# Performance work log

Measured on AMD Instinct MI355X. Metric: run time of the kernel, lower is better.

The kernel has to match this reference:

```python
import jax, jax.numpy as jnp
import numpy as np

K = 3          # kernel size
PAD = 1
STRIDE = 1
CIN = 256
COUT = 256


def _offset_conv(x, w, b):
    # standard 3x3 conv, NCHW / OIHW
    y = jax.lax.conv_general_dilated(
        x, w, window_strides=(STRIDE, STRIDE),
        padding=((PAD, PAD), (PAD, PAD)),
        dimension_numbers=("NCHW", "OIHW", "NCHW"))
    return y + b[None, :, None, None]


def _deform_conv2d(x, offset, weight):
    # x: [B,C,H,W], offset: [B,2*K*K,Ho,Wo] (y,x pairs, torchvision layout),
    # weight: [Cout,Cin,K,K]. No mask (deform-conv v1), zero padding.
    B, C, H, W = x.shape
    KK = K * K
    Ho, Wo = offset.shape[2], offset.shape[3]
    off = offset.reshape(B, KK, 2, Ho, Wo)
    dy, dx = off[:, :, 0], off[:, :, 1]                     # [B,KK,Ho,Wo]

    ky = jnp.repeat(jnp.arange(K), K).astype(x.dtype)       # [KK] kernel row
    kx = jnp.tile(jnp.arange(K), K).astype(x.dtype)         # [KK] kernel col
    base_y = (jnp.arange(Ho) * STRIDE - PAD).astype(x.dtype)
    base_x = (jnp.arange(Wo) * STRIDE - PAD).astype(x.dtype)

    py = base_y[None, None, :, None] + ky[None, :, None, None] + dy  # [B,KK,Ho,Wo]
    px = base_x[None, None, None, :] + kx[None, :, None, None] + dx

    y0 = jnp.floor(py); x0 = jnp.floor(px)
    y1 = y0 + 1.0;      x1 = x0 + 1.0
    wy1 = py - y0; wy0 = 1.0 - wy1
    wx1 = px - x0; wx0 = 1.0 - wx1

    xf = x.reshape(B, C, H * W)

    def gather(yi, xi):
        valid = ((yi >= 0) & (yi < H) & (xi >= 0) & (xi < W)).astype(x.dtype)
        yc = jnp.clip(yi, 0, H - 1).astype(jnp.int32)
        xc = jnp.clip(xi, 0, W - 1).astype(jnp.int32)
        idx = (yc * W + xc).reshape(B, -1)                  # [B, KK*Ho*Wo]
        v = jax.vmap(lambda xb, ib: xb[:, ib])(xf, idx)     # [B,C,KK*Ho*Wo]
        return v.reshape(B, C, KK, Ho, Wo), valid

    v00, m00 = gather(y0, x0)
    v01, m01 = gather(y0, x1)
    v10, m10 = gather(y1, x0)
    v11, m11 = gather(y1, x1)

    samp = (v00 * (wy0 * wx0 * m00)[:, None]
          + v01 * (wy0 * wx1 * m01)[:, None]
          + v10 * (wy1 * wx0 * m10)[:, None]
          + v11 * (wy1 * wx1 * m11)[:, None])               # [B,C,KK,Ho,Wo]

    w2 = weight.reshape(weight.shape[0], C, KK)             # [Cout,Cin,KK], KK=ky*K+kx
    return jnp.einsum('bckhw,ock->bohw', samp, w2)


def setup_inputs() -> dict:
    key = jax.random.key(0)
    k1, k2, k3, k4 = jax.random.split(key, 4)
    x = jax.random.normal(k1, (4, CIN, 64, 64), dtype=jnp.float32)
    # offset conv params (small init so sampled offsets are realistic)
    offset_w = jax.random.normal(k2, (2 * K * K, CIN, K, K), dtype=jnp.float32) * 0.01
    offset_b = jax.random.normal(k3, (2 * K * K,), dtype=jnp.float32) * 0.01
    # regular (deformable) conv weight; bias=False in the module
    weight = jax.random.normal(k4, (COUT, CIN, K, K), dtype=jnp.float32) * (1.0 / np.sqrt(CIN * K * K))
    return {"x": x, "offset_w": offset_w, "offset_b": offset_b, "weight": weight}


def reference(x, offset_w, offset_b, weight):
    offset = _offset_conv(x, offset_w, offset_b)
    return _deform_conv2d(x, offset, weight)
```

## Files before the change

### kernel.cpp

```cpp
#include <hip/hip_runtime.h>

#define CIN 256
#define COUT 256
#define Hh 64
#define Ww 64
#define Bb 4
#define HW 4096
#define NKK 9

typedef __attribute__((ext_vector_type(8))) short bf16x8;
typedef __attribute__((ext_vector_type(4))) float f32x4;

__device__ __forceinline__ unsigned short f2bf(float f) {
  unsigned int u = __builtin_bit_cast(unsigned int, f);
  unsigned int r = u + 0x7FFFu + ((u >> 16) & 1u);
  return (unsigned short)(r >> 16);
}
__device__ __forceinline__ float bf2f(unsigned short h) {
  unsigned int u = ((unsigned int)h) << 16;
  return __builtin_bit_cast(float, u);
}
__device__ __forceinline__ float bil(float2 f0, float2 f1, int eq, float4 w) {
  float t00 = eq ? f0.x : f0.y;
  float t01 = eq ? f0.y : f0.x;
  float t10 = eq ? f1.x : f1.y;
  float t11 = eq ? f1.y : f1.x;
  return t00 * w.x + t01 * w.y + t10 * w.z + t11 * w.w;
}

#define WB_ELEMS 589824
#define WOB_ELEMS 147456
#define OFFPART_FLOATS (Bb * 18 * HW)

__global__ __launch_bounds__(256) void prep_weights_kernel(
    const float* __restrict__ w, const float* __restrict__ ow,
    unsigned short* __restrict__ wBh, unsigned short* __restrict__ wBl,
    unsigned short* __restrict__ wOBh) {
  int i = blockIdx.x * 256 + threadIdx.x;
  if (i < WB_ELEMS) {
    int e = i & 7;
    int lane = (i >> 3) & 63;
    int ks = (i >> 9) & 1;
    int nt = (i >> 10) & 15;
    int cb = (i >> 14) & 3;
    int kk = i >> 16;
    int c = cb * 64 + ks * 32 + (lane >> 4) * 8 + e;
    int oc = nt * 16 + (lane & 15);
    float v = w[((size_t)oc * CIN + c) * 9 + kk];
    unsigned short hi = f2bf(v);
    wBh[i] = hi;
    wBl[i] = f2bf(v - bf2f(hi));
  } else {
    int j = i - WB_ELEMS;
    if (j < WOB_ELEMS) {
      int e = j & 7;
      int lane = (j >> 3) & 63;
      int ks = (j >> 9) & 1;
      int nt = (j >> 10) & 1;
      int cb = (j >> 11) & 3;
      int kk = j >> 13;
      int c = cb * 64 + ks * 32 + (lane >> 4) * 8 + e;
      int oc = nt * 16 + (lane & 15);
      float v = (oc < 18) ? ow[((size_t)oc * CIN + c) * 9 + kk] : 0.0f;
      wOBh[j] = f2bf(v);
    }
  }
}

__global__ __launch_bounds__(256) void offset_conv_kernel(
    const float* __restrict__ x,
    const unsigned short* __restrict__ wOBh,
    const float* __restrict__ ob,
    float* __restrict__ op0, float* __restrict__ op1) {
  __shared__ __align__(16) unsigned short smA[64 * 64];

  const int tid = threadIdx.x;
  const int bid = blockIdx.x;
  const int logical = (bid & 7) * 64 + (bid >> 3);
  const int chalf = logical & 1;
  const int rowid = logical >> 1;
  const int ho = rowid & 63;
  const int b  = rowid >> 6;
  const int lane = tid & 63;
  const int wv = tid >> 6;
  const int px = tid & 63;
  const int c8g = tid >> 6;

  f32x4 acc[2];
  #pragma unroll
  for (int n = 0; n < 2; ++n)
    #pragma unroll
    for (int q = 0; q < 4; ++q) acc[n][q] = 0.0f;

  const float* xb = x + (size_t)b * CIN * HW;

  for (int kk = 0; kk < NKK; ++kk) {
    int ky = kk / 3, kx = kk % 3;
    int y = ho - 1 + ky;
    if (y < 0 || y >= Hh) continue;
    int xx = px - 1 + kx;
    bool xv = (xx >= 0 && xx < Ww);
    int xxc = min(max(xx, 0), Ww - 1);
    const float* xrow = xb + (size_t)y * Ww + xxc;
    #pragma unroll
    for (int cb2 = 0; cb2 < 2; ++cb2) {
      int cb = chalf * 2 + cb2;
      __syncthreads();
      #pragma unroll
      for (int pass = 0; pass < 2; ++pass) {
        int c8 = c8g * 2 + pass;
        int cbase = cb * 64 + c8 * 8;
        unsigned int ph[4];
        #pragma unroll
        for (int j = 0; j < 4; ++j) {
          float v0 = xv ? xrow[(size_t)(cbase + 2 * j) * HW] : 0.0f;
          float v1 = xv ? xrow[(size_t)(cbase + 2 * j + 1) * HW] : 0.0f;
          ph[j] = (unsigned int)f2bf(v0) | ((unsigned int)f2bf(v1) << 16);
        }
        int boff = px * 128 + ((c8 ^ (px & 7)) * 16);
        *(uint4*)((char*)smA + boff) = make_uint4(ph[0], ph[1], ph[2], ph[3]);
      }
      __syncthreads();
      bf16x8 a[2];
      #pragma unroll
      for (int ks = 0; ks < 2; ++ks) {
        int pxa = wv * 16 + (lane & 15);
        int cg = ks * 4 + (lane >> 4);
        a[ks] = *(const bf16x8*)((const char*)smA + pxa * 128 + ((cg ^ (pxa & 7)) * 16));
      }
      bf16x8 wb[2][2];
      #pragma unroll
      for (int nt = 0; nt < 2; ++nt)
        #pragma unroll
        for (int ks = 0; ks < 2; ++ks) {
          size_t wi = ((((size_t)(kk * 4 + cb) * 2 + nt) * 2 + ks) * 64 + lane) * 8;
          wb[nt][ks] = *(const bf16x8*)(wOBh + wi);
        }
      #pragma unroll
      for (int nt = 0; nt < 2; ++nt)
        #pragma unroll
        for (int ks = 0; ks < 2; ++ks)
          acc[nt] = __builtin_amdgcn_mfma_f32_16x16x32_bf16(a[ks], wb[nt][ks], acc[nt], 0, 0, 0);
    }
  }
  float* opart = chalf ? op1 : op0;
  #pragma unroll
  for (int nt = 0; nt < 2; ++nt) {
    int oc = nt * 16 + (lane & 15);
    if (oc < 18) {
      float bias = chalf ? 0.0f : ob[oc];
      float4 v4 = make_float4(acc[nt][0] + bias, acc[nt][1] + bias,
                              acc[nt][2] + bias, acc[nt][3] + bias);
      int pxo = wv * 16 + (lane >> 4) * 4;
      *(float4*)(opart + ((size_t)b * 18 + oc) * HW + (size_t)ho * Ww + pxo) = v4;
    }
  }
}

__global__ __launch_bounds__(512, 2) void deform_main_kernel(
    const float* __restrict__ x,
    const float* __restrict__ op0, const float* __restrict__ op1,
    const unsigned short* __restrict__ wBh, const unsigned short* __restrict__ wBl,
    float* __restrict__ out) {
  __shared__ __align__(16) int4   sm_m[NKK][64];
  __shared__ __align__(16) float4 sm_w[NKK][64];
  __shared__ __align__(16) unsigned short smAh[2][64 * 64];
  __shared__ __align__(16) unsigned short smAl[2][64 * 64];

  const int tid = threadIdx.x;
  const int bid = blockIdx.x;
  const int blk = (bid & 7) * 32 + (bid >> 3);
  const int ho = blk & 63;
  const int b  = blk >> 6;
  const int lane = tid & 63;
  const int wv = tid >> 6;
  const int mh = wv >> 2;
  const int og = wv & 3;

  const float* ob0 = op0 + (size_t)b * 18 * HW + (size_t)ho * Ww;
  const float* ob1 = op1 + (size_t)b * 18 * HW + (size_t)ho * Ww;
  for (int i = tid; i < NKK * 64; i += 512) {
    int pp = i & 63;
    int kk = i >> 6;
    int ky = kk / 3, kx = kk % 3;
    float dy = ob0[(size_t)(2 * kk) * HW + pp] + ob1[(size_t)(2 * kk) * HW + pp];
    float dx = ob0[(size_t)(2 * kk + 1) * HW + pp] + ob1[(size_t)(2 * kk + 1) * HW + pp];
    float py = (float)(ho - 1 + ky) + dy;
    float pxf = (float)(pp - 1 + kx) + dx;
    float y0f = floorf(py), x0f = floorf(pxf);
    int y0 = (int)y0f, x0 = (int)x0f;
    float wy1 = py - y0f, wy0 = 1.0f - wy1;
    float wx1 = pxf - x0f, wx0 = 1.0f - wx1;
    float vy0 = (y0 >= 0 && y0 < Hh) ? 1.0f : 0.0f;
    float vy1 = (y0 + 1 >= 0 && y0 + 1 < Hh) ? 1.0f : 0.0f;
    float vx0 = (x0 >= 0 && x0 < Ww) ? 1.0f : 0.0f;
    float vx1 = (x0 + 1 >= 0 && x0 + 1 < Ww) ? 1.0f : 0.0f;
    int y0c = min(max(y0, 0), Hh - 1);
    int y1c = min(max(y0 + 1, 0), Hh - 1);
    int x0c = min(max(x0, 0), Ww - 2);
    int eq = (x0 == x0c) ? 1 : 0;
    sm_m[kk][pp] = make_int4(y0c * Ww + x0c, y1c * Ww + x0c, eq, 0);
    sm_w[kk][pp] = make_float4(wy0 * wx0 * vy0 * vx0, wy0 * wx1 * vy0 * vx1,
                               wy1 * wx0 * vy1 * vx0, wy1 * wx1 * vy1 * vx1);
  }
  __syncthreads();

  f32x4 acc[2][4];
  #pragma unroll
  for (int m = 0; m < 2; ++m)
    #pragma unroll
    for (int n = 0; n < 4; ++n)
      #pragma unroll
      for (int q = 0; q < 4; ++q) acc[m][n][q] = 0.0f;

  const float* xb = x + (size_t)b * CIN * HW;
  const int spx = tid & 63;
  const int sc8 = tid >> 6;
  const int sboff = spx * 128 + ((sc8 ^ (spx & 7)) * 16);

  {
    int4 ip = sm_m[0][spx];
    float4 wp = sm_w[0][spx];
    const float* xpB = xb + (size_t)(sc8 * 8) * HW;
    float2 g0[8], g1[8];
    #pragma unroll
    for (int j = 0; j < 8; ++j) {
      const float* xp = xpB + (size_t)j * HW;
      g0[j] = *(const float2*)(xp + ip.x);
      g1[j] = *(const float2*)(xp + ip.y);
    }
    unsigned int ph[4], pl[4];
    #pragma unroll
    for (int j2 = 0; j2 < 4; ++j2) {
      float v0 = bil(g0[2 * j2], g1[2 * j2], ip.z, wp);
      float v1 = bil(g0[2 * j2 + 1], g1[2 * j2 + 1], ip.z, wp);
      unsigned short h0 = f2bf(v0), h1 = f2bf(v1);
      ph[j2] = (unsigned int)h0 | ((unsigned int)h1 << 16);
      pl[j2] = (unsigned int)f2bf(v0 - bf2f(h0)) | ((unsigned int)f2bf(v1 - bf2f(h1)) << 16);
    }
    *(uint4*)((char*)smAh[0] + sboff) = make_uint4(ph[0], ph[1], ph[2], ph[3]);
    *(uint4*)((char*)smAl[0] + sboff) = make_uint4(pl[0], pl[1], pl[2], pl[3]);
  }
  __syncthreads();

  for (int ch = 0; ch < 36; ++ch) {
    const int cur = ch & 1;
    const int kk = ch >> 2, cb = ch & 3;

    bf16x8 ah[2][2], al[2][2];
    #pragma unroll
    for (int m = 0; m < 2; ++m)
      #pragma unroll
      for (int ks = 0; ks < 2; ++ks) {
        int pxa = mh * 32 + m * 16 + (lane & 15);
        int cg = ks * 4 + (lane >> 4);
        int aoff = pxa * 128 + ((cg ^ (pxa & 7)) * 16);
        ah[m][ks] = *(const bf16x8*)((const char*)smAh[cur] + aoff);
        al[m][ks] = *(const bf16x8*)((const char*)smAl[cur] + aoff);
      }

    bf16x8 wh[4][2], wl[4][2];
    #pragma unroll
    for (int nt = 0; nt < 4; ++nt)
      #pragma unroll
      for (int ks = 0; ks < 2; ++ks) {
        size_t wi = ((((size_t)(kk * 4 + cb) * 16 + (og * 4 + nt)) * 2 + ks) * 64 + lane) * 8;
        wh[nt][ks] = *(const bf16x8*)(wBh + wi);
        wl[nt][ks] = *(const bf16x8*)(wBl + wi);
      }
    asm volatile("" ::: "memory");

    float2 g0[8], g1[8];
    int4 ipn; float4 wpn;
    const bool have_next = (ch + 1 < 36);
    if (have_next) {
      int kkn = (ch + 1) >> 2, cbn = (ch + 1) & 3;
      ipn = sm_m[kkn][spx];
      wpn = sm_w[kkn][spx];
      const float* xpB = xb + (size_t)(cbn * 64 + sc8 * 8) * HW;
      #pragma unroll
      for (int j = 0; j < 8; ++j) {
        const float* xp = xpB + (size_t)j * HW;
        g0[j] = *(const float2*)(xp + ipn.x);
        g1[j] = *(const float2*)(xp + ipn.y);
      }
    }

    #pragma unroll
    for (int nt = 0; nt < 4; ++nt)
      #pragma unroll
      for (int ks = 0; ks < 2; ++ks) {
        acc[0][nt] = __builtin_amdgcn_mfma_f32_16x16x32_bf16(ah[0][ks], wh[nt][ks], acc[0][nt], 0, 0, 0);
        acc[1][nt] = __builtin_amdgcn_mfma_f32_16x16x32_bf16(ah[1][ks], wh[nt][ks], acc[1][nt], 0, 0, 0);
        acc[0][nt] = __builtin_amdgcn_mfma_f32_16x16x32_bf16(al[0][ks], wh[nt][ks], acc[0][nt], 0, 0, 0);
        acc[1][nt] = __builtin_amdgcn_mfma_f32_16x16x32_bf16(al[1][ks], wh[nt][ks], acc[1][nt], 0, 0, 0);
        acc[0][nt] = __builtin_amdgcn_mfma_f32_16x16x32_bf16(ah[0][ks], wl[nt][ks], acc[0][nt], 0, 0, 0);
        acc[1][nt] = __builtin_amdgcn_mfma_f32_16x16x32_bf16(ah[1][ks], wl[nt][ks], acc[1][nt], 0, 0, 0);
      }

    if (have_next) {
      unsigned int ph[4], pl[4];
      #pragma unroll
      for (int j2 = 0; j2 < 4; ++j2) {
        float v0 = bil(g0[2 * j2], g1[2 * j2], ipn.z, wpn);
        float v1 = bil(g0[2 * j2 + 1], g1[2 * j2 + 1], ipn.z, wpn);
        unsigned short h0 = f2bf(v0), h1 = f2bf(v1);
        ph[j2] = (unsigned int)h0 | ((unsigned int)h1 << 16);
        pl[j2] = (unsigned int)f2bf(v0 - bf2f(h0)) | ((unsigned int)f2bf(v1 - bf2f(h1)) << 16);
      }
      *(uint4*)((char*)smAh[cur ^ 1] + sboff) = make_uint4(ph[0], ph[1], ph[2], ph[3]);
      *(uint4*)((char*)smAl[cur ^ 1] + sboff) = make_uint4(pl[0], pl[1], pl[2], pl[3]);
    }
    __syncthreads();
  }

  #pragma unroll
  for (int m = 0; m < 2; ++m) {
    #pragma unroll
    for (int nt = 0; nt < 4; ++nt) {
      int oc = og * 64 + nt * 16 + (lane & 15);
      int pxo = mh * 32 + m * 16 + (lane >> 4) * 4;
      float4 v4 = make_float4(acc[m][nt][0], acc[m][nt][1], acc[m][nt][2], acc[m][nt][3]);
      *(float4*)(out + ((size_t)b * COUT + oc) * HW + (size_t)ho * Ww + pxo) = v4;
    }
  }
}

extern "C" void kernel_launch(void* const* d_in, const int* in_sizes, int n_in,
                              void* d_out, int out_size, void* d_ws, size_t ws_size,
                              hipStream_t stream) {
  const float* x  = (const float*)d_in[0];
  const float* ow = (const float*)d_in[1];
  const float* ob = (const float*)d_in[2];
  const float* w  = (const float*)d_in[3];
  float* out = (float*)d_out;

  float* op0 = (float*)d_ws;
  float* op1 = op0 + OFFPART_FLOATS;
  unsigned short* wBh  = (unsigned short*)(op1 + OFFPART_FLOATS);
  unsigned short* wBl  = wBh + WB_ELEMS;
  unsigned short* wOBh = wBl + WB_ELEMS;

  hipLaunchKernelGGL(prep_weights_kernel, dim3((WB_ELEMS + WOB_ELEMS) / 256),
                     dim3(256), 0, stream, w, ow, wBh, wBl, wOBh);
  hipLaunchKernelGGL(offset_conv_kernel, dim3(Bb * Hh * 2), dim3(256),
                     0, stream, x, wOBh, ob, op0, op1);
  hipLaunchKernelGGL(deform_main_kernel, dim3(Bb * Hh), dim3(512),
                     0, stream, x, op0, op1, wBh, wBl, out);
}
```

Before: 249.1 us.

## Remap waves to full-pixel tiles and hand-schedule loads with explicit waitcnt

Each of the eight waves now covers all 64 pixels and 32 output channels, instead of 32 pixels and 64 channels. This halves the per-wave weight-fragment global loads and doubles the LDS A-fragment reads. Weight and gather loads go through inline-asm global loads, with explicit s_waitcnt vmcnt counts and sched_barriers. The MFMAs can then start once the weight loads land, while the next chunk's gathers are still in flight. The risk is that hand-counted vmcnt values are fragile and could break if the compiler emits loads in a different order or count. The prologue gathers were also changed to scalar loads.

```diff
diff --git a/kernel.cpp b/kernel.cpp
--- a/kernel.cpp
+++ b/kernel.cpp
@@ -19,6 +19,16 @@
 __device__ __forceinline__ float bf2f(unsigned short h) {
   unsigned int u = ((unsigned int)h) << 16;
   return __builtin_bit_cast(float, u);
+}
+__device__ __forceinline__ bf16x8 gldx4(const void* p) {
+  bf16x8 r;
+  asm volatile("global_load_dwordx4 %0, %1, off" : "=&v"(r) : "v"(p));
+  return r;
+}
+__device__ __forceinline__ float2 gldx2(const void* p) {
+  float2 r;
+  asm volatile("global_load_dwordx2 %0, %1, off" : "=&v"(r) : "v"(p));
+  return r;
 }
 __device__ __forceinline__ float bil(float2 f0, float2 f1, int eq, float4 w) {
   float t00 = eq ? f0.x : f0.y;
@@ -173,9 +183,7 @@
   const int ho = blk & 63;
   const int b  = blk >> 6;
   const int lane = tid & 63;
-  const int wv = tid >> 6;
-  const int mh = wv >> 2;
-  const int og = wv & 3;
+  const int wvu = __builtin_amdgcn_readfirstlane(tid >> 6);
 
   const float* ob0 = op0 + (size_t)b * 18 * HW + (size_t)ho * Ww;
   const float* ob1 = op1 + (size_t)b * 18 * HW + (size_t)ho * Ww;
@@ -205,11 +213,11 @@
   }
   __syncthreads();
 
-  f32x4 acc[2][4];
+  f32x4 acc[4][2];
   #pragma unroll
-  for (int m = 0; m < 2; ++m)
-    #pragma unroll
-    for (int n = 0; n < 4; ++n)
+  for (int m = 0; m < 4; ++m)
+    #pragma unroll
+    for (int n = 0; n < 2; ++n)
       #pragma unroll
       for (int q = 0; q < 4; ++q) acc[m][n][q] = 0.0f;
 
@@ -222,18 +230,17 @@
     int4 ip = sm_m[0][spx];
     float4 wp = sm_w[0][spx];
     const float* xpB = xb + (size_t)(sc8 * 8) * HW;
-    float2 g0[8], g1[8];
-    #pragma unroll
-    for (int j = 0; j < 8; ++j) {
-      const float* xp = xpB + (size_t)j * HW;
-      g0[j] = *(const float2*)(xp + ip.x);
-      g1[j] = *(const float2*)(xp + ip.y);
-    }
     unsigned int ph[4], pl[4];
     #pragma unroll
     for (int j2 = 0; j2 < 4; ++j2) {
-      float v0 = bil(g0[2 * j2], g1[2 * j2], ip.z, wp);
-      float v1 = bil(g0[2 * j2 + 1], g1[2 * j2 + 1], ip.z, wp);
+      const float* xq0 = xpB + (size_t)(2 * j2) * HW;
+      const float* xq1 = xpB + (size_t)(2 * j2 + 1) * HW;
+      float2 a0 = make_float2(xq0[ip.x], xq0[ip.x + 1]);
+      float2 a1 = make_float2(xq0[ip.y], xq0[ip.y + 1]);
+      float2 b0 = make_float2(xq1[ip.x], xq1[ip.x + 1]);
+      float2 b1 = make_float2(xq1[ip.y], xq1[ip.y + 1]);
+      float v0 = bil(a0, a1, ip.z, wp);
+      float v1 = bil(b0, b1, ip.z, wp);
       unsigned short h0 = f2bf(v0), h1 = f2bf(v1);
       ph[j2] = (unsigned int)h0 | ((unsigned int)h1 << 16);
       pl[j2] = (unsigned int)f2bf(v0 - bf2f(h0)) | ((unsigned int)f2bf(v1 - bf2f(h1)) << 16);
@@ -246,33 +253,32 @@
   for (int ch = 0; ch < 36; ++ch) {
     const int cur = ch & 1;
     const int kk = ch >> 2, cb = ch & 3;
-
-    bf16x8 ah[2][2], al[2][2];
-    #pragma unroll
-    for (int m = 0; m < 2; ++m)
+    const bool have_next = (ch + 1 < 36);
+
+    bf16x8 ah[4][2], al[4][2];
+    #pragma unroll
+    for (int m = 0; m < 4; ++m)
       #pragma unroll
       for (int ks = 0; ks < 2; ++ks) {
-        int pxa = mh * 32 + m * 16 + (lane & 15);
+        int pxa = m * 16 + (lane & 15);
         int cg = ks * 4 + (lane >> 4);
         int aoff = pxa * 128 + ((cg ^ (pxa & 7)) * 16);
         ah[m][ks] = *(const bf16x8*)((const char*)smAh[cur] + aoff);
         al[m][ks] = *(const bf16x8*)((const char*)smAl[cur] + aoff);
       }
 
-    bf16x8 wh[4][2], wl[4][2];
-    #pragma unroll
-    for (int nt = 0; nt < 4; ++nt)
+    bf16x8 wh[2][2], wl[2][2];
+    #pragma unroll
+    for (int nt = 0; nt < 2; ++nt)
       #pragma unroll
       for (int ks = 0; ks < 2; ++ks) {
-        size_t wi = ((((size_t)(kk * 4 + cb) * 16 + (og * 4 + nt)) * 2 + ks) * 64 + lane) * 8;
-        wh[nt][ks] = *(const bf16x8*)(wBh + wi);
-        wl[nt][ks] = *(const bf16x8*)(wBl + wi);
-      }
-    asm volatile("" ::: "memory");
+        size_t wi = ((((size_t)(kk * 4 + cb) * 16 + (wvu * 2 + nt)) * 2 + ks) * 64 + lane) * 8;
+        wh[nt][ks] = gldx4(wBh + wi);
+        wl[nt][ks] = gldx4(wBl + wi);
+      }
 
     float2 g0[8], g1[8];
     int4 ipn; float4 wpn;
-    const bool have_next = (ch + 1 < 36);
     if (have_next) {
       int kkn = (ch + 1) >> 2, cbn = (ch + 1) & 3;
       ipn = sm_m[kkn][spx];
@@ -281,24 +287,29 @@
       #pragma unroll
       for (int j = 0; j < 8; ++j) {
         const float* xp = xpB + (size_t)j * HW;
-        g0[j] = *(const float2*)(xp + ipn.x);
-        g1[j] = *(const float2*)(xp + ipn.y);
-      }
-    }
-
-    #pragma unroll
-    for (int nt = 0; nt < 4; ++nt)
-      #pragma unroll
-      for (int ks = 0; ks < 2; ++ks) {
-        acc[0][nt] = __builtin_amdgcn_mfma_f32_16x16x32_bf16(ah[0][ks], wh[nt][ks], acc[0][nt], 0, 0, 0);
-        acc[1][nt] = __builtin_amdgcn_mfma_f32_16x16x32_bf16(ah[1][ks], wh[nt][ks], acc[1][nt], 0, 0, 0);
-        acc[0][nt] = __builtin_amdgcn_mfma_f32_16x16x32_bf16(al[0][ks], wh[nt][ks], acc[0][nt], 0, 0, 0);
-        acc[1][nt] = __builtin_amdgcn_mfma_f32_16x16x32_bf16(al[1][ks], wh[nt][ks], acc[1][nt], 0, 0, 0);
-        acc[0][nt] = __builtin_amdgcn_mfma_f32_16x16x32_bf16(ah[0][ks], wl[nt][ks], acc[0][nt], 0, 0, 0);
-        acc[1][nt] = __builtin_amdgcn_mfma_f32_16x16x32_bf16(ah[1][ks], wl[nt][ks], acc[1][nt], 0, 0, 0);
-      }
+        g0[j] = gldx2(xp + ipn.x);
+        g1[j] = gldx2(xp + ipn.y);
+      }
+    }
+
+    if (have_next) { asm volatile("s_waitcnt vmcnt(16)" ::: "memory"); }
+    else           { asm volatile("s_waitcnt vmcnt(0)"  ::: "memory"); }
+    __builtin_amdgcn_sched_barrier(0);
+
+    #pragma unroll
+    for (int m = 0; m < 4; ++m)
+      #pragma unroll
+      for (int nt = 0; nt < 2; ++nt)
+        #pragma unroll
+        for (int ks = 0; ks < 2; ++ks) {
+          acc[m][nt] = __builtin_amdgcn_mfma_f32_16x16x32_bf16(ah[m][ks], wh[nt][ks], acc[m][nt], 0, 0, 0);
+          acc[m][nt] = __builtin_amdgcn_mfma_f32_16x16x32_bf16(al[m][ks], wh[nt][ks], acc[m][nt], 0, 0, 0);
+          acc[m][nt] = __builtin_amdgcn_mfma_f32_16x16x32_bf16(ah[m][ks], wl[nt][ks], acc[m][nt], 0, 0, 0);
+        }
 
     if (have_next) {
+      asm volatile("s_waitcnt vmcnt(0)" ::: "memory");
+      __builtin_amdgcn_sched_barrier(0);
       unsigned int ph[4], pl[4];
       #pragma unroll
       for (int j2 = 0; j2 < 4; ++j2) {
@@ -315,11 +326,11 @@
   }
 
   #pragma unroll
-  for (int m = 0; m < 2; ++m) {
-    #pragma unroll
-    for (int nt = 0; nt < 4; ++nt) {
-      int oc = og * 64 + nt * 16 + (lane & 15);
-      int pxo = mh * 32 + m * 16 + (lane >> 4) * 4;
+  for (int m = 0; m < 4; ++m) {
+    #pragma unroll
+    for (int nt = 0; nt < 2; ++nt) {
+      int oc = wvu * 32 + nt * 16 + (lane & 15);
+      int pxo = m * 16 + (lane >> 4) * 4;
       float4 v4 = make_float4(acc[m][nt][0], acc[m][nt][1], acc[m][nt][2], acc[m][nt][3]);
       *(float4*)(out + ((size_t)b * COUT + oc) * HW + (size_t)ho * Ww + pxo) = v4;
     }
```

New measurement: 210.5 us. 15.5% less time.
